# Kernel tuning notes

Measured on AMD Instinct MI355X. Metric: run time of the kernel, lower is better.

The kernel has to match this reference:

```python
import jax, jax.numpy as jnp
import numpy as np

GAMMA = 0.99
NUM_QUANTILES = 50
STEP_TYPE_LAST = 2
HUBER_DELTA = 1.0

T, B, Q = 128, 512, NUM_QUANTILES


def setup_inputs() -> dict:
    key = jax.random.key(0)
    k1, k2, k3, k4, k5 = jax.random.split(key, 5)
    return {
        "reward": jax.random.normal(k1, (T, B), dtype=jnp.float32),
        "step_type": jax.random.randint(k2, (T, B), 0, 3, dtype=jnp.int32),
        "discount": jax.random.uniform(k3, (T, B), dtype=jnp.float32),
        "value": jax.random.normal(k4, (T, B, Q), dtype=jnp.float32),
        "target_value": jax.random.normal(k5, (T, B, Q), dtype=jnp.float32),
    }


def discounted_return(rewards, values, step_types, discounts):
    """alf value_ops.discounted_return: backward-in-time recurrence.

    rewards/step_types/discounts: [T, B]; values: [T, B, Q].
    Returns [T-1, B, Q]. rets[T-1]=values[T-1];
    rets[t] = is_last[t]*values[t] + (1-is_last[t])*(discounts[t+1]*rets[t+1] + rewards[t+1]).
    """
    is_last = (step_types == STEP_TYPE_LAST).astype(values.dtype)[..., None]  # [T,B,1]
    r = rewards[..., None]    # [T,B,1]
    d = discounts[..., None]  # [T,B,1]

    def step(carry, xs):
        is_last_t, v_t, r_tp1, d_tp1 = xs
        acc = carry * d_tp1 + r_tp1
        ret = is_last_t * v_t + (1.0 - is_last_t) * acc
        return ret, ret

    init = values[-1]
    xs = (is_last[:-1], values[:-1], r[1:], d[1:])
    _, rets = jax.lax.scan(step, init, xs, reverse=True)
    return rets  # [T-1, B, Q]


def huber(x):
    ax = jnp.abs(x)
    return jnp.where(ax <= HUBER_DELTA, 0.5 * x * x, HUBER_DELTA * (ax - 0.5 * HUBER_DELTA))


def reference(reward, step_type, discount, value, target_value):
    # td_lambda == 1.0 -> full discounted return (computed with no grad / detached)
    returns = jax.lax.stop_gradient(
        discounted_return(reward, target_value, step_type, discount * GAMMA))  # [T-1,B,Q]
    v = value[:-1]  # [T-1,B,Q]

    q = returns.shape[-1]
    tau = (jnp.arange(q, dtype=value.dtype) + 0.5) / q  # [Q] cdf midpoints

    # diff[..., i, j] = target_quantile_i - estimated_quantile_j
    diff = returns[..., :, None] - v[..., None, :]  # [T-1,B,Qt,Qe]
    weight = jnp.abs(tau - (jax.lax.stop_gradient(diff) < 0).astype(diff.dtype))
    loss = weight * huber(diff)
    # sum_over_quantiles=True: mean over target quantiles, sum over estimate quantiles
    loss = loss.mean(axis=-2).sum(axis=-1)  # [T-1,B]
    # tensor_extend_zero: append a zero row for the last time step -> [T,B]
    loss = jnp.concatenate([loss, jnp.zeros_like(loss[-1:])], axis=0)
    return loss
```

## Files before the change

kernel.cpp:

```cpp
#include <hip/hip_runtime.h>

#define GAMMA 0.99f
constexpr int T_DIM = 128;
constexpr int B_DIM = 512;
constexpr int Q_DIM = 50;
constexpr int NROW  = (T_DIM - 1) * B_DIM;
constexpr int NPAIR = NROW * Q_DIM;
constexpr int SLOT  = 52;
constexpr int LROWS = 7;
constexpr int KEEP  = -1;

__global__ void __launch_bounds__(128) coeff_kernel(
    const float* __restrict__ reward,
    const int*   __restrict__ step_type,
    const float* __restrict__ discount,
    float* __restrict__ alpha,
    float* __restrict__ beta,
    int*   __restrict__ anchor) {
  __shared__ float sp[128], sqa[128], sqb[128];
  __shared__ int   snv[128];
  const int t = threadIdx.x;
  const int b = blockIdx.x;

  float p, qa, qb; int nv;
  if (t < T_DIM - 1) {
    const bool  last = (step_type[t * B_DIM + b] == 2);
    const float d    = GAMMA * discount[(t + 1) * B_DIM + b];
    const float r    = reward[(t + 1) * B_DIM + b];
    p  = last ? 0.0f : d;
    qa = last ? 1.0f : 0.0f;
    qb = last ? 0.0f : r;
    nv = last ? t    : KEEP;
  } else {
    p = 1.0f; qa = 0.0f; qb = 0.0f; nv = KEEP;
  }
  sp[t] = p; sqa[t] = qa; sqb[t] = qb; snv[t] = nv;
  __syncthreads();

#pragma unroll
  for (int off = 1; off < 128; off <<= 1) {
    const bool act = (t + off) < 128;
    float p2 = 1.0f, qa2 = 0.0f, qb2 = 0.0f; int nv2 = KEEP;
    if (act) { p2 = sp[t+off]; qa2 = sqa[t+off]; qb2 = sqb[t+off]; nv2 = snv[t+off]; }
    __syncthreads();
    if (act) {
      qa = fmaf(p, qa2, qa);
      qb = fmaf(p, qb2, qb);
      p  = p * p2;
      nv = (nv == KEEP) ? nv2 : nv;
      sp[t] = p; sqa[t] = qa; sqb[t] = qb; snv[t] = nv;
    }
    __syncthreads();
  }

  if (t < T_DIM - 1) {
    const int row = (b << 7) + t;
    alpha[row]  = p + qa;
    beta[row]   = qb;
    anchor[row] = (nv == KEEP) ? (T_DIM - 1) : nv;
  }
}

__global__ void __launch_bounds__(256) loss_kernel(
    const float* __restrict__ value,
    const float* __restrict__ tv,
    const float* __restrict__ alpha,
    const float* __restrict__ beta,
    const int*   __restrict__ anchor,
    float*       __restrict__ out) {
  __shared__ __align__(16) float sret[LROWS * SLOT];

  const int tid  = threadIdx.x;
  const int idx0 = blockIdx.x * 256;
  const int r0   = idx0 / Q_DIM;

  for (int e = tid; e < LROWS * Q_DIM; e += 256) {
    const int lr  = e / Q_DIM;
    const int i   = e - lr * Q_DIM;
    const int row = r0 + lr;
    if (row < NROW) {
      const int b = row & (B_DIM - 1);
      const int t = row >> 9;
      const int ci = (b << 7) + t;
      const int n = anchor[ci];
      const float rv =
          fmaf(alpha[ci], tv[(n * B_DIM + b) * Q_DIM + i], beta[ci]);
      sret[lr * SLOT + i] = rv;
    }
  }
  __syncthreads();

  const int   idx  = idx0 + tid;
  const int   row  = idx / Q_DIM;
  const int   j    = idx - row * Q_DIM;
  const int   lr   = row - r0;
  const float v    = value[idx];
  const float tm05 = ((float)j + 0.5f) * (1.0f / Q_DIM) - 0.5f;

  const float* rp = &sret[lr * SLOT];
  float s = 0.0f;

  auto pair = [&](float reti) {
    const float d  = reti - v;
    const float c  = __builtin_amdgcn_fmed3f(d, -1.0f, 1.0f);
    const float u  = fmaf(-0.5f, fabsf(c), fabsf(d));
    const float in = fmaf(0.5f, fabsf(c), tm05 * c);
    s = fmaf(u, in, s);
  };

#pragma unroll
  for (int i0 = 0; i0 < 48; i0 += 4) {
    const float4 rr = *reinterpret_cast<const float4*>(rp + i0);
    pair(rr.x); pair(rr.y); pair(rr.z); pair(rr.w);
  }
  {
    const float2 rr = *reinterpret_cast<const float2*>(rp + 48);
    pair(rr.x); pair(rr.y);
  }

  const int r_lo = __builtin_amdgcn_readlane(row, 0);
  const int r_hi = __builtin_amdgcn_readlane(row, 63);
  float s_lo  = (row == r_lo) ? s : 0.0f;
  float s_hi  = (row == r_hi) ? s : 0.0f;
  float s_tot = s;
#pragma unroll
  for (int off = 32; off > 0; off >>= 1) {
    s_lo  += __shfl_xor(s_lo,  off, 64);
    s_hi  += __shfl_xor(s_hi,  off, 64);
    s_tot += __shfl_xor(s_tot, off, 64);
  }

  if ((tid & 63) == 0) {
    const float k = 1.0f / Q_DIM;
    if (r_hi == r_lo) {
      atomicAdd(out + r_lo, s_tot * k);
    } else {
      atomicAdd(out + r_lo, s_lo * k);
      atomicAdd(out + r_hi, s_hi * k);
      if (r_hi > r_lo + 1)
        out[r_lo + 1] = (s_tot - s_lo - s_hi) * k;
    }
  }
}

extern "C" void kernel_launch(void* const* d_in, const int* in_sizes, int n_in,
                              void* d_out, int out_size, void* d_ws, size_t ws_size,
                              hipStream_t stream) {
  const float* reward       = (const float*)d_in[0];
  const int*   step_type    = (const int*)  d_in[1];
  const float* discount     = (const float*)d_in[2];
  const float* value        = (const float*)d_in[3];
  const float* target_value = (const float*)d_in[4];
  float* out = (float*)d_out;

  float* alpha  = (float*)d_ws;
  float* beta   = alpha + B_DIM * 128;
  int*   anchor = (int*)(beta + B_DIM * 128);

  hipMemsetAsync(out, 0, (size_t)T_DIM * B_DIM * sizeof(float), stream);

  coeff_kernel<<<B_DIM, 128, 0, stream>>>(reward, step_type, discount,
                                          alpha, beta, anchor);

  loss_kernel<<<NPAIR / 256, 256, 0, stream>>>(value, target_value,
                                               alpha, beta, anchor, out);
}
```

Before: 114.0 us.

## Row-align loss blocks, reduce per-row in shared memory, drop memset and atomics

Each loss block now covers 20 whole rows. 250 threads each compute pairwise losses for 4 rows, and per-column partial sums are reduced through shared memory, one wavefront per group of 5 rows. Because every output row is written exactly once, the atomics and the separate memset are no longer needed; the last time-step row is zeroed inside the coeff kernel instead. The cost is fewer blocks, 6 idle lanes per block, and an extra shared-memory pass and barrier.

```diff
diff --git a/kernel.cpp b/kernel.cpp
--- a/kernel.cpp
+++ b/kernel.cpp
@@ -5,10 +5,10 @@
 constexpr int B_DIM = 512;
 constexpr int Q_DIM = 50;
 constexpr int NROW  = (T_DIM - 1) * B_DIM;
-constexpr int NPAIR = NROW * Q_DIM;
 constexpr int SLOT  = 52;
-constexpr int LROWS = 7;
+constexpr int R_BLK = 20;
 constexpr int KEEP  = -1;
+constexpr int GRID_LOSS = (NROW + R_BLK - 1) / R_BLK;
 
 __global__ void __launch_bounds__(128) coeff_kernel(
     const float* __restrict__ reward,
@@ -16,7 +16,8 @@
     const float* __restrict__ discount,
     float* __restrict__ alpha,
     float* __restrict__ beta,
-    int*   __restrict__ anchor) {
+    int*   __restrict__ anchor,
+    float* __restrict__ out) {
   __shared__ float sp[128], sqa[128], sqb[128];
   __shared__ int   snv[128];
   const int t = threadIdx.x;
@@ -33,6 +34,7 @@
     nv = last ? t    : KEEP;
   } else {
     p = 1.0f; qa = 0.0f; qb = 0.0f; nv = KEEP;
+    out[(T_DIM - 1) * B_DIM + b] = 0.0f;
   }
   sp[t] = p; sqa[t] = qa; sqb[t] = qb; snv[t] = nv;
   __syncthreads();
@@ -68,78 +70,74 @@
     const float* __restrict__ beta,
     const int*   __restrict__ anchor,
     float*       __restrict__ out) {
-  __shared__ __align__(16) float sret[LROWS * SLOT];
+  __shared__ __align__(16) float sret[R_BLK * SLOT];
+  __shared__ float pacc[R_BLK * SLOT];
 
-  const int tid  = threadIdx.x;
-  const int idx0 = blockIdx.x * 256;
-  const int r0   = idx0 / Q_DIM;
+  const int tid = threadIdx.x;
+  const int r0  = blockIdx.x * R_BLK;
 
-  for (int e = tid; e < LROWS * Q_DIM; e += 256) {
+  for (int e = tid; e < R_BLK * Q_DIM; e += 256) {
     const int lr  = e / Q_DIM;
     const int i   = e - lr * Q_DIM;
     const int row = r0 + lr;
+    float rv = 0.0f;
     if (row < NROW) {
-      const int b = row & (B_DIM - 1);
-      const int t = row >> 9;
+      const int b  = row & (B_DIM - 1);
+      const int t  = row >> 9;
       const int ci = (b << 7) + t;
-      const int n = anchor[ci];
-      const float rv =
-          fmaf(alpha[ci], tv[(n * B_DIM + b) * Q_DIM + i], beta[ci]);
-      sret[lr * SLOT + i] = rv;
+      const int n  = anchor[ci];
+      rv = fmaf(alpha[ci], tv[(n * B_DIM + b) * Q_DIM + i], beta[ci]);
+    }
+    sret[lr * SLOT + i] = rv;
+  }
+  __syncthreads();
+
+  const bool act   = tid < 5 * Q_DIM;
+  const int  r_off = tid / Q_DIM;
+  const int  j     = tid - r_off * Q_DIM;
+  const float tm05 = ((float)j + 0.5f) * (1.0f / Q_DIM) - 0.5f;
+
+  if (act) {
+#pragma unroll
+    for (int rb = 0; rb < 4; ++rb) {
+      const int lr = rb * 5 + r_off;
+      const float* rp = &sret[lr * SLOT];
+      const float v = value[(r0 + rb * 5) * Q_DIM + tid];
+
+      float s = 0.0f;
+      auto pair = [&](float reti) {
+        const float d  = reti - v;
+        const float c  = __builtin_amdgcn_fmed3f(d, -1.0f, 1.0f);
+        const float u  = fmaf(-0.5f, fabsf(c), fabsf(d));
+        const float in = fmaf(0.5f, fabsf(c), tm05 * c);
+        s = fmaf(u, in, s);
+      };
+#pragma unroll
+      for (int i0 = 0; i0 < 48; i0 += 4) {
+        const float4 rr = *reinterpret_cast<const float4*>(rp + i0);
+        pair(rr.x); pair(rr.y); pair(rr.z); pair(rr.w);
+      }
+      {
+        const float2 rr = *reinterpret_cast<const float2*>(rp + 48);
+        pair(rr.x); pair(rr.y);
+      }
+      pacc[lr * SLOT + j] = s;
     }
   }
   __syncthreads();
 
-  const int   idx  = idx0 + tid;
-  const int   row  = idx / Q_DIM;
-  const int   j    = idx - row * Q_DIM;
-  const int   lr   = row - r0;
-  const float v    = value[idx];
-  const float tm05 = ((float)j + 0.5f) * (1.0f / Q_DIM) - 0.5f;
-
-  const float* rp = &sret[lr * SLOT];
-  float s = 0.0f;
-
-  auto pair = [&](float reti) {
-    const float d  = reti - v;
-    const float c  = __builtin_amdgcn_fmed3f(d, -1.0f, 1.0f);
-    const float u  = fmaf(-0.5f, fabsf(c), fabsf(d));
-    const float in = fmaf(0.5f, fabsf(c), tm05 * c);
-    s = fmaf(u, in, s);
-  };
-
+  const int w    = tid >> 6;
+  const int lane = tid & 63;
 #pragma unroll
-  for (int i0 = 0; i0 < 48; i0 += 4) {
-    const float4 rr = *reinterpret_cast<const float4*>(rp + i0);
-    pair(rr.x); pair(rr.y); pair(rr.z); pair(rr.w);
-  }
-  {
-    const float2 rr = *reinterpret_cast<const float2*>(rp + 48);
-    pair(rr.x); pair(rr.y);
-  }
-
-  const int r_lo = __builtin_amdgcn_readlane(row, 0);
-  const int r_hi = __builtin_amdgcn_readlane(row, 63);
-  float s_lo  = (row == r_lo) ? s : 0.0f;
-  float s_hi  = (row == r_hi) ? s : 0.0f;
-  float s_tot = s;
+  for (int k = 0; k < 5; ++k) {
+    const int lr   = w * 5 + k;
+    const int grow = r0 + lr;
+    float x = (lane < Q_DIM) ? pacc[lr * SLOT + lane] : 0.0f;
 #pragma unroll
-  for (int off = 32; off > 0; off >>= 1) {
-    s_lo  += __shfl_xor(s_lo,  off, 64);
-    s_hi  += __shfl_xor(s_hi,  off, 64);
-    s_tot += __shfl_xor(s_tot, off, 64);
-  }
-
-  if ((tid & 63) == 0) {
-    const float k = 1.0f / Q_DIM;
-    if (r_hi == r_lo) {
-      atomicAdd(out + r_lo, s_tot * k);
-    } else {
-      atomicAdd(out + r_lo, s_lo * k);
-      atomicAdd(out + r_hi, s_hi * k);
-      if (r_hi > r_lo + 1)
-        out[r_lo + 1] = (s_tot - s_lo - s_hi) * k;
-    }
+    for (int off = 32; off > 0; off >>= 1)
+      x += __shfl_xor(x, off, 64);
+    if (lane == 0 && grow < NROW)
+      out[grow] = x * (1.0f / Q_DIM);
   }
 }
 
@@ -157,11 +155,9 @@
   float* beta   = alpha + B_DIM * 128;
   int*   anchor = (int*)(beta + B_DIM * 128);
 
-  hipMemsetAsync(out, 0, (size_t)T_DIM * B_DIM * sizeof(float), stream);
+  coeff_kernel<<<B_DIM, 128, 0, stream>>>(reward, step_type, discount,
+                                          alpha, beta, anchor, out);
 
-  coeff_kernel<<<B_DIM, 128, 0, stream>>>(reward, step_type, discount,
-                                          alpha, beta, anchor);
-
-  loss_kernel<<<NPAIR / 256, 256, 0, stream>>>(value, target_value,
-                                               alpha, beta, anchor, out);
+  loss_kernel<<<GRID_LOSS, 256, 0, stream>>>(value, target_value,
+                                             alpha, beta, anchor, out);
 }
```

New measurement: 105.2 us. 1.08x faster.
